# Performance work log

Hardware: AMD Instinct MI355X
Metric: run time of the kernel (lower is better)

## Reference

```python
import jax, jax.numpy as jnp
import numpy as np


def setup_inputs() -> dict:
    key = jax.random.key(0)
    ks = jax.random.split(key, 8)
    B, S, H = 4, 2048, 1024
    heads = 16
    lim = 1.0 / np.sqrt(H)  # nn.Linear default init range
    x = jax.random.normal(ks[0], (B, S, H), dtype=jnp.float32)
    atten_mask = jnp.zeros((B, 1, S, 1), dtype=jnp.float32)  # 1.0 marks padded positions
    Wq = jax.random.uniform(ks[1], (H, H), jnp.float32, -lim, lim)
    bq = jax.random.uniform(ks[2], (H,), jnp.float32, -lim, lim)
    Wk = jax.random.uniform(ks[3], (H, H), jnp.float32, -lim, lim)
    bk = jax.random.uniform(ks[4], (H,), jnp.float32, -lim, lim)
    Wv = jax.random.uniform(ks[5], (H, H), jnp.float32, -lim, lim)
    bv = jax.random.uniform(ks[6], (H,), jnp.float32, -lim, lim)
    return {"x": x, "Wq": Wq, "bq": bq, "Wk": Wk, "bk": bk, "Wv": Wv, "bv": bv,
            "atten_mask": atten_mask, "attention_head_num": 16}


def reference(x, Wq, bq, Wk, bk, Wv, bv, atten_mask, attention_head_num):
    B, S, H = x.shape
    h = attention_head_num
    d = H // h
    # QKV projections (torch Linear: x @ W.T + b)
    q = (x @ Wq.T + bq).reshape(B, S, h, d).transpose(0, 2, 1, 3)  # [B,h,S,d]
    k = (x @ Wk.T + bk).reshape(B, S, h, d).transpose(0, 2, 1, 3)
    v = (x @ Wv.T + bv).reshape(B, S, h, d).transpose(0, 2, 1, 3)
    # combined padding + look-ahead mask: True -> masked
    causal = jnp.triu(jnp.ones((S, S), dtype=atten_mask.dtype), 1)  # [S,S]
    mask = (atten_mask + causal) >= 1.0  # [B,1 or h,S,S] broadcast
    mask = jnp.broadcast_to(mask, (B, h, S, S))
    scale = 1.0 / jnp.sqrt(jnp.asarray(d, dtype=jnp.float32))
    scores = jnp.einsum('bhqd,bhkd->bhqk', q, k) * scale
    scores = jnp.where(mask, jnp.float32(-1e9), scores)
    att = jax.nn.softmax(scores, axis=-1)
    out = jnp.einsum('bhqk,bhkd->bhqd', att, v)  # [B,h,S,d]
    return out.transpose(0, 2, 1, 3).reshape(B, S, H)
```

## Files before the change

### kernel.cpp

```cpp
#include <hip/hip_runtime.h>
#include <hip/hip_bf16.h>
#include <stdint.h>

typedef short v8s __attribute__((ext_vector_type(8)));
typedef float v4f __attribute__((ext_vector_type(4)));
typedef unsigned long long u64;
typedef unsigned short u16;
typedef unsigned int u32;
typedef u64 v2u __attribute__((ext_vector_type(2)));

__device__ __forceinline__ u16 f2bf(float f) {
    unsigned u = __builtin_bit_cast(unsigned, f);
    u += 0x7FFFu + ((u >> 16) & 1u);
    return (u16)(u >> 16);
}

__device__ __forceinline__ u32 cvt_pk_bf16(float lo, float hi) {
    u32 r;
    asm("v_cvt_pk_bf16_f32 %0, %1, %2" : "=v"(r) : "v"(lo), "v"(hi));
    return r;
}

__device__ __forceinline__ float ex2(float x) {
    float r;
    asm("v_exp_f32 %0, %1" : "=v"(r) : "v"(x));
    return r;
}

__device__ __forceinline__ void gload_lds16(const void* g, const void* lds) {
    __builtin_amdgcn_global_load_lds(
        (const __attribute__((address_space(1))) unsigned int*)(unsigned long long)g,
        (__attribute__((address_space(3))) unsigned int*)(unsigned int)(unsigned long long)lds,
        16, 0, 0);
}

__global__ __launch_bounds__(256) void cvt_all(const float* __restrict__ x,
                                               const float* __restrict__ wq,
                                               const float* __restrict__ wk,
                                               const float* __restrict__ wv,
                                               u16* __restrict__ xb, u16* __restrict__ wqb,
                                               u16* __restrict__ wkb, u16* __restrict__ wvb) {
    int i = blockIdx.x * 256 + threadIdx.x;
    const float* in;
    u16* out;
    if (i < 2097152)      { in = x;  out = xb; }
    else if (i < 2359296) { in = wq; out = wqb; i -= 2097152; }
    else if (i < 2621440) { in = wk; out = wkb; i -= 2359296; }
    else                  { in = wv; out = wvb; i -= 2621440; }
    float4 v = ((const float4*)in)[i];
    ((ushort4*)out)[i] = make_ushort4(f2bf(v.x), f2bf(v.y), f2bf(v.z), f2bf(v.w));
}

__global__ __launch_bounds__(256, 4)
void qkv_gemm_all(const u16* __restrict__ X,
                  const u16* __restrict__ Wq, const u16* __restrict__ Wk, const u16* __restrict__ Wv,
                  const float* __restrict__ bq, const float* __restrict__ bk, const float* __restrict__ bv,
                  u16* __restrict__ Qg, u16* __restrict__ Kg, u16* __restrict__ VTg) {
    __shared__ __align__(16) char smem[34816];
    char* ldsA = smem;
    char* ldsB = smem + 16384;
    u16*  ldsE = (u16*)smem;

    const int l = (blockIdx.x & 7) * 192 + (blockIdx.x >> 3);
    const int mode = l >> 9;
    const int bx = l & 511;
    const u16* W = (mode == 0) ? Wq : (mode == 1) ? Wk : Wv;
    const float* bias = (mode == 0) ? bq : (mode == 1) ? bk : bv;
    u16* Out = (mode == 0) ? Qg : (mode == 1) ? Kg : VTg;

    const int t = threadIdx.x;
    const int lane = t & 63, wave = t >> 6;
    const int lhi = lane >> 4, llo = lane & 15;
    const int wm = wave >> 1, wn = wave & 1;
    const int m0 = (bx >> 3) * 128;
    const int n0 = (bx & 7) * 128;

    const int srow = (t * 16) >> 7;
    const int ssc = ((t * 16) >> 4) & 7;
    v4f acc[4][4] = {};

    for (int k0 = 0; k0 < 1024; k0 += 64) {
        #pragma unroll
        for (int i = 0; i < 4; ++i) {
            int row = i * 32 + srow;
            int c = ssc ^ (row & 7);
            const char* wbaseA = ldsA + (i * 256 + wave * 64) * 16;
            const char* wbaseB = ldsB + (i * 256 + wave * 64) * 16;
            gload_lds16(X + (m0 + row) * 1024 + k0 + c * 8, wbaseA);
            gload_lds16(W + (n0 + row) * 1024 + k0 + c * 8, wbaseB);
        }
        __syncthreads();
        __builtin_amdgcn_s_setprio(1);
        #pragma unroll
        for (int s = 0; s < 2; ++s) {
            v8s af[4], bf[4];
            #pragma unroll
            for (int i = 0; i < 4; ++i) {
                int r = wm * 64 + i * 16 + llo;
                af[i] = *(const v8s*)(ldsA + r * 128 + (((lhi + 4 * s) ^ (r & 7)) << 4));
            }
            #pragma unroll
            for (int j = 0; j < 4; ++j) {
                int r = wn * 64 + j * 16 + llo;
                bf[j] = *(const v8s*)(ldsB + r * 128 + (((lhi + 4 * s) ^ (r & 7)) << 4));
            }
            #pragma unroll
            for (int i = 0; i < 4; ++i)
                #pragma unroll
                for (int j = 0; j < 4; ++j)
                    acc[i][j] = __builtin_amdgcn_mfma_f32_16x16x32_bf16(af[i], bf[j], acc[i][j], 0, 0, 0);
        }
        __builtin_amdgcn_s_setprio(0);
        __syncthreads();
    }

    float bv_[4];
    #pragma unroll
    for (int j = 0; j < 4; ++j) bv_[j] = bias[n0 + wn * 64 + j * 16 + llo];
    const float scl = (mode == 0) ? 0.18033688011112042f : 1.0f;

    #pragma unroll
    for (int i = 0; i < 4; ++i) {
        #pragma unroll
        for (int j = 0; j < 4; ++j) {
            #pragma unroll
            for (int r = 0; r < 4; ++r) {
                int ml = wm * 64 + i * 16 + lhi * 4 + r;
                int nl = wn * 64 + j * 16 + llo;
                float v = (acc[i][j][r] + bv_[j]) * scl;
                u16 hh = f2bf(v);
                if (mode == 2) ldsE[nl * 136 + ml] = hh;
                else           ldsE[ml * 136 + nl] = hh;
            }
        }
    }
    __syncthreads();

    const int row = t >> 1, half = t & 1;
    if (mode == 2) {
        int n = n0 + row, hh = n >> 6, dd = n & 63;
        int b = m0 >> 11, sbase = (m0 & 2047) + half * 64;
        u16* dst = Out + ((b * 16 + hh) * 64 + dd) * 2048 + sbase;
        #pragma unroll
        for (int j = 0; j < 8; ++j)
            *(v8s*)(dst + j * 8) = *(const v8s*)&ldsE[row * 136 + half * 64 + j * 8];
    } else {
        int m = m0 + row, b = m >> 11, s = m & 2047;
        int hh = (n0 + half * 64) >> 6;
        u16* dst = Out + ((b * 16 + hh) * 2048 + s) * 64;
        #pragma unroll
        for (int j = 0; j < 8; ++j)
            *(v8s*)(dst + j * 8) = *(const v8s*)&ldsE[row * 136 + half * 64 + j * 8];
    }
}

__global__ __launch_bounds__(256, 3)
void flash_attn(const u16* __restrict__ Qg, const u16* __restrict__ Kg,
                const u16* __restrict__ VTg, const float* __restrict__ am,
                float* __restrict__ out) {
    __shared__ __align__(16) char smem[41472];
    char* ldsK = smem;
    char* ldsV = smem + 16384;
    char* ldsP = smem + 32768 + (threadIdx.x >> 6) * 2176;

    const int t = threadIdx.x;
    const int lane = t & 63, wave = t >> 6;
    const int lhi = lane >> 4, llo = lane & 15;
    const int bh = blockIdx.x;
    const int qi = 31 - blockIdx.y;
    const int b = bh >> 4, h = bh & 15;
    const int qw = qi * 64 + wave * 16;
    const int q = qw + llo;

    v8s qf[2];
    #pragma unroll
    for (int s = 0; s < 2; ++s)
        qf[s] = *(const v8s*)(Qg + (bh * 2048 + q) * 64 + lhi * 8 + 32 * s);

    const float rowpen = am[b * 2048 + q];

    const int srow = (t * 16) >> 7, ssc = ((t * 16) >> 4) & 7;
    const int sc1 = ssc ^ (srow & 7), sc2 = ssc ^ ((srow + 32) & 7);
    #define STAGE(buf, kj2) do {                                                   \
        const int kv0_ = (kj2) * 64;                                               \
        const char* wbK = ldsK + (buf) * 8192 + (wave * 64) * 16;                  \
        const char* wbV = ldsV + (buf) * 8192 + (wave * 64) * 16;                  \
        gload_lds16(Kg + (bh * 2048 + kv0_ + srow) * 64 + sc1 * 8, wbK);           \
        gload_lds16(VTg + (bh * 64 + srow) * 2048 + kv0_ + sc1 * 8, wbV);          \
        gload_lds16(Kg + (bh * 2048 + kv0_ + srow + 32) * 64 + sc2 * 8, wbK + 4096); \
        gload_lds16(VTg + (bh * 64 + srow + 32) * 2048 + kv0_ + sc2 * 8, wbV + 4096); \
    } while (0)

    float mrow = -1e30f, lrow = 0.f;
    v4f o_acc[4] = {};

    STAGE(0, 0);
    __syncthreads();

    for (int kj = 0; kj <= qi; ++kj) {
        const int cur = kj & 1;
        if (kj < qi) STAGE(cur ^ 1, kj + 1);
        const char* K = ldsK + cur * 8192;
        const char* V = ldsV + cur * 8192;
        const int kv0 = kj * 64;

        const int nt4 = (kj == qi) ? (wave + 1) : 4;
        v4f sacc[4] = {};
        __builtin_amdgcn_s_setprio(1);
        #pragma unroll
        for (int tt = 0; tt < 4; ++tt) {
            if (tt < nt4) {
                #pragma unroll
                for (int s = 0; s < 2; ++s) {
                    int row = tt * 16 + llo;
                    int c = lhi + 4 * s;
                    v8s kb = *(const v8s*)(K + row * 128 + ((c ^ (row & 7)) << 4));
                    sacc[tt] = __builtin_amdgcn_mfma_f32_16x16x32_bf16(kb, qf[s], sacc[tt], 0, 0, 0);
                }
            }
        }
        __builtin_amdgcn_s_setprio(0);

        if (kj == qi) {
            #pragma unroll
            for (int tt = 0; tt < 4; ++tt)
                #pragma unroll
                for (int r = 0; r < 4; ++r) {
                    int kvg = kv0 + tt * 16 + lhi * 4 + r;
                    if (kvg > q) sacc[tt][r] = -1e30f;
                }
        }
        if (rowpen >= 1.0f) {
            #pragma unroll
            for (int tt = 0; tt < 4; ++tt)
                #pragma unroll
                for (int r = 0; r < 4; ++r) sacc[tt][r] = -1e30f;
        }

        float lmx = fmaxf(fmaxf(sacc[0][0], sacc[0][1]), fmaxf(sacc[0][2], sacc[0][3]));
        #pragma unroll
        for (int tt = 1; tt < 4; ++tt)
            lmx = fmaxf(lmx, fmaxf(fmaxf(sacc[tt][0], sacc[tt][1]), fmaxf(sacc[tt][2], sacc[tt][3])));

        if (__any(lmx > mrow + 8.0f)) {
            float mx = fmaxf(lmx, __shfl_xor(lmx, 16));
            mx = fmaxf(mx, __shfl_xor(mx, 32));
            const float mn = fmaxf(mrow, mx);
            const float sc_o = ex2(mrow - mn);
            mrow = mn;
            lrow *= sc_o;
            #pragma unroll
            for (int dt = 0; dt < 4; ++dt)
                #pragma unroll
                for (int r = 0; r < 4; ++r) o_acc[dt][r] *= sc_o;
        }

        float rs = 0.f;
        #pragma unroll
        for (int tt = 0; tt < 4; ++tt) {
            float p0 = ex2(sacc[tt][0] - mrow);
            float p1 = ex2(sacc[tt][1] - mrow);
            float p2 = ex2(sacc[tt][2] - mrow);
            float p3 = ex2(sacc[tt][3] - mrow);
            rs += (p0 + p1) + (p2 + p3);
            u32 w0 = cvt_pk_bf16(p0, p1);
            u32 w1 = cvt_pk_bf16(p2, p3);
            *(u64*)(ldsP + llo * 136 + tt * 32 + lhi * 8) = (u64)w0 | ((u64)w1 << 32);
        }
        rs += __shfl_xor(rs, 16);
        rs += __shfl_xor(rs, 32);
        lrow += rs;

        __builtin_amdgcn_s_setprio(1);
        #pragma unroll
        for (int s = 0; s < 2; ++s) {
            u64 plo = *(const u64*)(ldsP + llo * 136 + lhi * 16 + s * 64);
            u64 phi = *(const u64*)(ldsP + llo * 136 + lhi * 16 + s * 64 + 8);
            v2u tmp; tmp.x = plo; tmp.y = phi;
            v8s pb = __builtin_bit_cast(v8s, tmp);
            #pragma unroll
            for (int dt = 0; dt < 4; ++dt) {
                int vrow = dt * 16 + llo;
                v8s vb = *(const v8s*)(V + vrow * 128 + (((lhi + 4 * s) ^ (vrow & 7)) << 4));
                o_acc[dt] = __builtin_amdgcn_mfma_f32_16x16x32_bf16(vb, pb, o_acc[dt], 0, 0, 0);
            }
        }
        __builtin_amdgcn_s_setprio(0);
        __syncthreads();
    }

    const float inv = 1.0f / lrow;
    float* dst = out + (size_t)(b * 2048 + q) * 1024 + h * 64 + lhi * 4;
    #pragma unroll
    for (int dt = 0; dt < 4; ++dt) {
        float4 o;
        o.x = o_acc[dt][0] * inv;
        o.y = o_acc[dt][1] * inv;
        o.z = o_acc[dt][2] * inv;
        o.w = o_acc[dt][3] * inv;
        *(float4*)(dst + dt * 16) = o;
    }
}

extern "C" void kernel_launch(void* const* d_in, const int* in_sizes, int n_in,
                              void* d_out, int out_size, void* d_ws, size_t ws_size,
                              hipStream_t stream) {
    const float* x  = (const float*)d_in[0];
    const float* Wq = (const float*)d_in[1];
    const float* bq = (const float*)d_in[2];
    const float* Wk = (const float*)d_in[3];
    const float* bk = (const float*)d_in[4];
    const float* Wv = (const float*)d_in[5];
    const float* bv = (const float*)d_in[6];
    const float* amask = (const float*)d_in[7];
    float* out = (float*)d_out;

    char* ws = (char*)d_ws;
    u16* xb  = (u16*)(ws);
    u16* Wqb = (u16*)(ws + 16777216);
    u16* Wkb = (u16*)(ws + 16777216 + 2097152);
    u16* Wvb = (u16*)(ws + 16777216 + 2 * 2097152);
    u16* Qg  = (u16*)(ws + 23068672);
    u16* Kg  = (u16*)(ws + 39845888);
    u16* VTg = (u16*)(ws + 56623104);

    cvt_all<<<11264, 256, 0, stream>>>(x, Wq, Wk, Wv, xb, Wqb, Wkb, Wvb);
    qkv_gemm_all<<<1536, 256, 0, stream>>>(xb, Wqb, Wkb, Wvb, bq, bk, bv, Qg, Kg, VTg);
    flash_attn<<<dim3(64, 32), 256, 0, stream>>>(Qg, Kg, VTg, amask, out);
}
```

Before: 158.2 us.

## Use 128-query blocks with 8 waves sharing each staged K/V tile

The flash-attention block grows from 4 to 8 waves, so each block covers 128 query rows and every staged 64-key K/V tile is reused by twice as many waves. This halves global K/V traffic per query and the number of blocks. Each wave skips fully masked key tiles and applies the causal mask only on diagonal tiles. The per-row sum reduction across lanes is moved out of the loop to a single final shuffle. In exchange, waves in the lower half of a block idle at block-wide barriers while the upper half still processes tiles, and launch bounds raise register pressure.

After: 206.4 us. +30.5%, slower.

```diff
diff --git a/kernel.cpp b/kernel.cpp
--- a/kernel.cpp
+++ b/kernel.cpp
@@ -154,11 +154,11 @@
     }
 }
 
-__global__ __launch_bounds__(256, 3)
+__global__ __launch_bounds__(512, 4)
 void flash_attn(const u16* __restrict__ Qg, const u16* __restrict__ Kg,
                 const u16* __restrict__ VTg, const float* __restrict__ am,
                 float* __restrict__ out) {
-    __shared__ __align__(16) char smem[41472];
+    __shared__ __align__(16) char smem[50176];
     char* ldsK = smem;
     char* ldsV = smem + 16384;
     char* ldsP = smem + 32768 + (threadIdx.x >> 6) * 2176;
@@ -166,10 +166,10 @@
     const int t = threadIdx.x;
     const int lane = t & 63, wave = t >> 6;
     const int lhi = lane >> 4, llo = lane & 15;
-    const int bh = blockIdx.x;
-    const int qi = 31 - blockIdx.y;
+    const int qi = 15 - blockIdx.x;
+    const int bh = blockIdx.y;
     const int b = bh >> 4, h = bh & 15;
-    const int qw = qi * 64 + wave * 16;
+    const int qw = qi * 128 + wave * 16;
     const int q = qw + llo;
 
     v8s qf[2];
@@ -179,117 +179,119 @@
 
     const float rowpen = am[b * 2048 + q];
 
-    const int srow = (t * 16) >> 7, ssc = ((t * 16) >> 4) & 7;
-    const int sc1 = ssc ^ (srow & 7), sc2 = ssc ^ ((srow + 32) & 7);
+    const int srow = t >> 3;
+    const int scol = (t & 7) ^ (srow & 7);
     #define STAGE(buf, kj2) do {                                                   \
         const int kv0_ = (kj2) * 64;                                               \
-        const char* wbK = ldsK + (buf) * 8192 + (wave * 64) * 16;                  \
-        const char* wbV = ldsV + (buf) * 8192 + (wave * 64) * 16;                  \
-        gload_lds16(Kg + (bh * 2048 + kv0_ + srow) * 64 + sc1 * 8, wbK);           \
-        gload_lds16(VTg + (bh * 64 + srow) * 2048 + kv0_ + sc1 * 8, wbV);          \
-        gload_lds16(Kg + (bh * 2048 + kv0_ + srow + 32) * 64 + sc2 * 8, wbK + 4096); \
-        gload_lds16(VTg + (bh * 64 + srow + 32) * 2048 + kv0_ + sc2 * 8, wbV + 4096); \
+        const char* wbK = ldsK + (buf) * 8192 + wave * 1024;                       \
+        const char* wbV = ldsV + (buf) * 8192 + wave * 1024;                       \
+        gload_lds16(Kg + (bh * 2048 + kv0_ + srow) * 64 + scol * 8, wbK);          \
+        gload_lds16(VTg + (bh * 64 + srow) * 2048 + kv0_ + scol * 8, wbV);         \
     } while (0)
 
-    float mrow = -1e30f, lrow = 0.f;
+    float mrow = -1e30f, lsum = 0.f;
     v4f o_acc[4] = {};
 
+    const int ntiles = 2 * qi + 2;
     STAGE(0, 0);
     __syncthreads();
 
-    for (int kj = 0; kj <= qi; ++kj) {
+    for (int kj = 0; kj < ntiles; ++kj) {
         const int cur = kj & 1;
-        if (kj < qi) STAGE(cur ^ 1, kj + 1);
+        if (kj + 1 < ntiles) STAGE(cur ^ 1, kj + 1);
         const char* K = ldsK + cur * 8192;
         const char* V = ldsV + cur * 8192;
         const int kv0 = kj * 64;
 
-        const int nt4 = (kj == qi) ? (wave + 1) : 4;
-        v4f sacc[4] = {};
-        __builtin_amdgcn_s_setprio(1);
-        #pragma unroll
-        for (int tt = 0; tt < 4; ++tt) {
-            if (tt < nt4) {
-                #pragma unroll
-                for (int s = 0; s < 2; ++s) {
-                    int row = tt * 16 + llo;
-                    int c = lhi + 4 * s;
-                    v8s kb = *(const v8s*)(K + row * 128 + ((c ^ (row & 7)) << 4));
-                    sacc[tt] = __builtin_amdgcn_mfma_f32_16x16x32_bf16(kb, qf[s], sacc[tt], 0, 0, 0);
+        if (kv0 <= qw + 15) {
+            const int nt4 = min(4, ((qw + 15 - kv0) >> 4) + 1);
+
+            v4f sacc[4] = {};
+            __builtin_amdgcn_s_setprio(1);
+            #pragma unroll
+            for (int tt = 0; tt < 4; ++tt) {
+                if (tt < nt4) {
+                    #pragma unroll
+                    for (int s = 0; s < 2; ++s) {
+                        int row = tt * 16 + llo;
+                        int c = lhi + 4 * s;
+                        v8s kb = *(const v8s*)(K + row * 128 + ((c ^ (row & 7)) << 4));
+                        sacc[tt] = __builtin_amdgcn_mfma_f32_16x16x32_bf16(kb, qf[s], sacc[tt], 0, 0, 0);
+                    }
                 }
             }
+            __builtin_amdgcn_s_setprio(0);
+
+            if (kv0 + 63 > qw) {
+                #pragma unroll
+                for (int tt = 0; tt < 4; ++tt)
+                    #pragma unroll
+                    for (int r = 0; r < 4; ++r) {
+                        int kvg = kv0 + tt * 16 + lhi * 4 + r;
+                        if (kvg > q) sacc[tt][r] = -1e30f;
+                    }
+            }
+            if (rowpen >= 1.0f) {
+                #pragma unroll
+                for (int tt = 0; tt < 4; ++tt)
+                    #pragma unroll
+                    for (int r = 0; r < 4; ++r) sacc[tt][r] = -1e30f;
+            }
+
+            float lmx = fmaxf(fmaxf(sacc[0][0], sacc[0][1]), fmaxf(sacc[0][2], sacc[0][3]));
+            #pragma unroll
+            for (int tt = 1; tt < 4; ++tt)
+                lmx = fmaxf(lmx, fmaxf(fmaxf(sacc[tt][0], sacc[tt][1]), fmaxf(sacc[tt][2], sacc[tt][3])));
+
+            if (__any(lmx > mrow + 8.0f)) {
+                float mx = fmaxf(lmx, __shfl_xor(lmx, 16));
+                mx = fmaxf(mx, __shfl_xor(mx, 32));
+                const float mn = fmaxf(mrow, mx);
+                const float sc_o = ex2(mrow - mn);
+                mrow = mn;
+                lsum *= sc_o;
+                #pragma unroll
+                for (int dt = 0; dt < 4; ++dt)
+                    #pragma unroll
+                    for (int r = 0; r < 4; ++r) o_acc[dt][r] *= sc_o;
+            }
+
+            float rs = 0.f;
+            #pragma unroll
+            for (int tt = 0; tt < 4; ++tt) {
+                float p0 = ex2(sacc[tt][0] - mrow);
+                float p1 = ex2(sacc[tt][1] - mrow);
+                float p2 = ex2(sacc[tt][2] - mrow);
+                float p3 = ex2(sacc[tt][3] - mrow);
+                rs += (p0 + p1) + (p2 + p3);
+                u32 w0 = cvt_pk_bf16(p0, p1);
+                u32 w1 = cvt_pk_bf16(p2, p3);
+                *(u64*)(ldsP + llo * 136 + tt * 32 + lhi * 8) = (u64)w0 | ((u64)w1 << 32);
+            }
+            lsum += rs;
+
+            __builtin_amdgcn_s_setprio(1);
+            #pragma unroll
+            for (int s = 0; s < 2; ++s) {
+                u64 plo = *(const u64*)(ldsP + llo * 136 + lhi * 16 + s * 64);
+                u64 phi = *(const u64*)(ldsP + llo * 136 + lhi * 16 + s * 64 + 8);
+                v2u tmp; tmp.x = plo; tmp.y = phi;
+                v8s pb = __builtin_bit_cast(v8s, tmp);
+                #pragma unroll
+                for (int dt = 0; dt < 4; ++dt) {
+                    int vrow = dt * 16 + llo;
+                    v8s vb = *(const v8s*)(V + vrow * 128 + (((lhi + 4 * s) ^ (vrow & 7)) << 4));
+                    o_acc[dt] = __builtin_amdgcn_mfma_f32_16x16x32_bf16(vb, pb, o_acc[dt], 0, 0, 0);
+                }
+            }
+            __builtin_amdgcn_s_setprio(0);
         }
-        __builtin_amdgcn_s_setprio(0);
-
-        if (kj == qi) {
-            #pragma unroll
-            for (int tt = 0; tt < 4; ++tt)
-                #pragma unroll
-                for (int r = 0; r < 4; ++r) {
-                    int kvg = kv0 + tt * 16 + lhi * 4 + r;
-                    if (kvg > q) sacc[tt][r] = -1e30f;
-                }
-        }
-        if (rowpen >= 1.0f) {
-            #pragma unroll
-            for (int tt = 0; tt < 4; ++tt)
-                #pragma unroll
-                for (int r = 0; r < 4; ++r) sacc[tt][r] = -1e30f;
-        }
-
-        float lmx = fmaxf(fmaxf(sacc[0][0], sacc[0][1]), fmaxf(sacc[0][2], sacc[0][3]));
-        #pragma unroll
-        for (int tt = 1; tt < 4; ++tt)
-            lmx = fmaxf(lmx, fmaxf(fmaxf(sacc[tt][0], sacc[tt][1]), fmaxf(sacc[tt][2], sacc[tt][3])));
-
-        if (__any(lmx > mrow + 8.0f)) {
-            float mx = fmaxf(lmx, __shfl_xor(lmx, 16));
-            mx = fmaxf(mx, __shfl_xor(mx, 32));
-            const float mn = fmaxf(mrow, mx);
-            const float sc_o = ex2(mrow - mn);
-            mrow = mn;
-            lrow *= sc_o;
-            #pragma unroll
-            for (int dt = 0; dt < 4; ++dt)
-                #pragma unroll
-                for (int r = 0; r < 4; ++r) o_acc[dt][r] *= sc_o;
-        }
-
-        float rs = 0.f;
-        #pragma unroll
-        for (int tt = 0; tt < 4; ++tt) {
-            float p0 = ex2(sacc[tt][0] - mrow);
-            float p1 = ex2(sacc[tt][1] - mrow);
-            float p2 = ex2(sacc[tt][2] - mrow);
-            float p3 = ex2(sacc[tt][3] - mrow);
-            rs += (p0 + p1) + (p2 + p3);
-            u32 w0 = cvt_pk_bf16(p0, p1);
-            u32 w1 = cvt_pk_bf16(p2, p3);
-            *(u64*)(ldsP + llo * 136 + tt * 32 + lhi * 8) = (u64)w0 | ((u64)w1 << 32);
-        }
-        rs += __shfl_xor(rs, 16);
-        rs += __shfl_xor(rs, 32);
-        lrow += rs;
-
-        __builtin_amdgcn_s_setprio(1);
-        #pragma unroll
-        for (int s = 0; s < 2; ++s) {
-            u64 plo = *(const u64*)(ldsP + llo * 136 + lhi * 16 + s * 64);
-            u64 phi = *(const u64*)(ldsP + llo * 136 + lhi * 16 + s * 64 + 8);
-            v2u tmp; tmp.x = plo; tmp.y = phi;
-            v8s pb = __builtin_bit_cast(v8s, tmp);
-            #pragma unroll
-            for (int dt = 0; dt < 4; ++dt) {
-                int vrow = dt * 16 + llo;
-                v8s vb = *(const v8s*)(V + vrow * 128 + (((lhi + 4 * s) ^ (vrow & 7)) << 4));
-                o_acc[dt] = __builtin_amdgcn_mfma_f32_16x16x32_bf16(vb, pb, o_acc[dt], 0, 0, 0);
-            }
-        }
-        __builtin_amdgcn_s_setprio(0);
         __syncthreads();
     }
 
-    const float inv = 1.0f / lrow;
+    lsum += __shfl_xor(lsum, 16);
+    lsum += __shfl_xor(lsum, 32);
+    const float inv = 1.0f / lsum;
     float* dst = out + (size_t)(b * 2048 + q) * 1024 + h * 64 + lhi * 4;
     #pragma unroll
     for (int dt = 0; dt < 4; ++dt) {
@@ -326,5 +328,5 @@
 
     cvt_all<<<11264, 256, 0, stream>>>(x, Wq, Wk, Wv, xb, Wqb, Wkb, Wvb);
     qkv_gemm_all<<<1536, 256, 0, stream>>>(xb, Wqb, Wkb, Wvb, bq, bk, bv, Qg, Kg, VTg);
-    flash_attn<<<dim3(64, 32), 256, 0, stream>>>(Qg, Kg, VTg, amask, out);
-}
+    flash_attn<<<dim3(16, 64), 512, 0, stream>>>(Qg, Kg, VTg, amask, out);
+}
```
